# Performance work log

Hardware: AMD Instinct MI355X
Metric: run time of the kernel (lower is better)

The kernel has to match this reference:

```python
import jax, jax.numpy as jnp
import numpy as np

D_MODEL = 256
D_STATE = 16
D_CONV = 3
D_INNER = 512   # expand(2.0) * d_model
DT_RANK = 16    # ceil(d_model / 16)
BATCH = 4
SEQLEN = 2048


def setup_inputs() -> dict:
    key = jax.random.key(0)
    ks = jax.random.split(key, 8)
    s = 0.02
    x = jax.random.normal(ks[0], (BATCH, D_MODEL, SEQLEN), jnp.float32)
    W_in = jax.random.normal(ks[1], (2 * D_INNER, D_MODEL), jnp.float32) * s
    W_dw = jax.random.normal(ks[2], (D_INNER, 1, D_CONV), jnp.float32) * 0.3
    b_dw = jnp.zeros((D_INNER,), jnp.float32)
    W_x = jax.random.normal(ks[3], (DT_RANK + 2 * D_STATE, D_INNER), jnp.float32) * s
    W_dt = jax.random.normal(ks[4], (D_INNER, DT_RANK), jnp.float32) * s
    # bias so softplus(delta) stays small/stable, like mamba dt init
    b_dt = jax.random.normal(ks[5], (D_INNER,), jnp.float32) * 0.5 - 4.0
    A_log = jnp.log(jnp.broadcast_to(
        jnp.arange(1, D_STATE + 1, dtype=jnp.float32), (D_INNER, D_STATE)))
    D = jnp.ones((D_INNER,), jnp.float32)
    W_out = jax.random.normal(ks[6], (D_MODEL, D_INNER), jnp.float32) * s
    return {"x": x, "W_in": W_in, "W_dw": W_dw, "b_dw": b_dw, "W_x": W_x,
            "W_dt": W_dt, "b_dt": b_dt, "A_log": A_log, "D": D, "W_out": W_out}


def reference(x, W_in, W_dw, b_dw, W_x, W_dt, b_dt, A_log, D, W_out):
    residual = x
    # in_proj: 1x1 conv == per-position GEMM -> (B, 2*d_inner, L)
    xz = jnp.einsum('cd,bdl->bcl', W_in, x)
    u, z = jnp.split(xz, 2, axis=1)                       # each (B, d_inner, L)
    # depthwise conv1d, 'same' padding (pad = d_conv//2)
    u = jax.lax.conv_general_dilated(
        u, W_dw, window_strides=(1,), padding=[(D_CONV // 2, D_CONV // 2)],
        dimension_numbers=('NCH', 'OIH', 'NCH'), feature_group_count=D_INNER)
    u = jax.nn.silu(u + b_dw[None, :, None])
    # x_proj -> dt (low rank), B_ssm, C_ssm
    x_dbl = jnp.einsum('cd,bdl->bcl', W_x, u)             # (B, dt_rank+2N, L)
    dt_lr = x_dbl[:, :DT_RANK]                            # (B, dt_rank, L)
    B_ssm = x_dbl[:, DT_RANK:DT_RANK + D_STATE]           # (B, N, L)
    C_ssm = x_dbl[:, DT_RANK + D_STATE:]                  # (B, N, L)
    delta = jax.nn.softplus(
        jnp.einsum('dr,brl->bdl', W_dt, dt_lr) + b_dt[None, :, None])
    A = -jnp.exp(A_log)                                   # (d_inner, N)
    # discretized transition / input, laid out scan-major: (L, B, d_inner, N)
    dA = jnp.exp(jnp.einsum('bdl,dn->lbdn', delta, A))
    dBu = jnp.einsum('bdl,bnl,bdl->lbdn', delta, B_ssm, u)
    C_t = jnp.transpose(C_ssm, (2, 0, 1))                 # (L, B, N)
    h0 = jnp.zeros((x.shape[0], D_INNER, D_STATE), jnp.float32)

    def step(h, inp):
        dA_t, dBu_t, c_t = inp
        h = dA_t * h + dBu_t                              # (B, d_inner, N)
        y_t = jnp.einsum('bdn,bn->bd', h, c_t)            # (B, d_inner)
        return h, y_t

    _, ys = jax.lax.scan(step, h0, (dA, dBu, C_t))        # ys: (L, B, d_inner)
    y = jnp.transpose(ys, (1, 2, 0)) + D[None, :, None] * u
    y = y * jax.nn.silu(z)
    return jnp.einsum('od,bdl->bol', W_out, y) + residual
```

## Files before the change

### kernel.cpp

```cpp
#include <hip/hip_runtime.h>
#include <math.h>

#define DM 256
#define DI 512
#define BB 4
#define LL 2048
#define NC 64
#define CH (LL / NC)

typedef short bf16x8 __attribute__((ext_vector_type(8)));
typedef float f32x4 __attribute__((ext_vector_type(4)));
typedef unsigned short u16;

__device__ inline u16 f2bf(float f) {
    union { float f; unsigned u; } v;
    v.f = f;
    return (u16)((v.u + 0x7FFF + ((v.u >> 16) & 1)) >> 16);
}
__device__ inline float bf2f(u16 h) {
    union { unsigned u; float f; } v;
    v.u = ((unsigned)h) << 16;
    return v.f;
}

__global__ __launch_bounds__(256) void k_prep(const float* __restrict__ x,
                                              const float* __restrict__ W_in,
                                              const float* __restrict__ W_out,
                                              const float* __restrict__ W_x,
                                              u16* __restrict__ xt,
                                              u16* __restrict__ wbf_in,
                                              u16* __restrict__ wbf_out,
                                              u16* __restrict__ wbf_x) {
    const int bid = blockIdx.x;
    const int t = threadIdx.x;
    if (bid < 512) {
        __shared__ float tile[64][65];
        const int lb = bid & 31, mb = (bid >> 5) & 3, b = bid >> 7;
        const int m0 = mb * 64, l0 = lb * 64;
        const float* xb = x + ((size_t)b * DM + m0) * LL + l0;
#pragma unroll
        for (int i = 0; i < 16; i++) {
            int idx = t + i * 256;
            int r = idx >> 6, c = idx & 63;
            tile[r][c] = xb[(size_t)r * LL + c];
        }
        __syncthreads();
        u16* ob = xt + ((size_t)b * LL + l0) * DM + m0;
#pragma unroll
        for (int i = 0; i < 16; i++) {
            int idx = t + i * 256;
            int r = idx >> 6, c = idx & 63;
            ob[(size_t)r * DM + c] = f2bf(tile[c][r]);
        }
        return;
    }
    const float* src;
    u16* dst;
    int i4;
    if (bid < 768) { src = W_in; dst = wbf_in; i4 = (bid - 512) * 256 + t; }
    else if (bid < 896) { src = W_out; dst = wbf_out; i4 = (bid - 768) * 256 + t; }
    else { src = W_x; dst = wbf_x; i4 = (bid - 896) * 256 + t; }
    float4 v = ((const float4*)src)[i4];
    unsigned o0 = (unsigned)f2bf(v.x) | ((unsigned)f2bf(v.y) << 16);
    unsigned o1 = (unsigned)f2bf(v.z) | ((unsigned)f2bf(v.w) << 16);
    ((uint2*)dst)[i4] = make_uint2(o0, o1);
}

__global__ __launch_bounds__(256) void k_gemm_in(const u16* __restrict__ xt,
                                                 const u16* __restrict__ Wb,
                                                 u16* __restrict__ xz) {
    __shared__ short As[128 * 64];
    __shared__ short Bs[128 * 64];
    const int b = blockIdx.z;
    const int l0 = blockIdx.x * 128;
    const int c0 = blockIdx.y * 128;
    const int t = threadIdx.x;
    const int lane = t & 63, wv = t >> 6;
    const int wr = wv >> 1, wc = wv & 1;
    const u16* xb = xt + (size_t)b * LL * DM;
    f32x4 acc[4][4] = {};
    for (int k0 = 0; k0 < DM; k0 += 64) {
#pragma unroll
        for (int i = 0; i < 4; i++) {
            int ci = t + i * 256;
            int r = ci >> 3;
            int cb = (ci & 7) * 16;
            int pd = r * 128 + (cb ^ ((r & 7) << 4));
            *(float4*)((char*)As + pd) =
                *(const float4*)((const char*)(xb + (size_t)(l0 + r) * DM + k0) + cb);
            *(float4*)((char*)Bs + pd) =
                *(const float4*)((const char*)(Wb + (size_t)(c0 + r) * DM + k0) + cb);
        }
        __syncthreads();
#pragma unroll
        for (int kk = 0; kk < 2; kk++) {
            const int lcb = kk * 64 + (lane >> 4) * 16;
            bf16x8 af[4], bfr[4];
#pragma unroll
            for (int mi = 0; mi < 4; mi++) {
                int r = wr * 64 + mi * 16 + (lane & 15);
                af[mi] = *(const bf16x8*)((const char*)As + r * 128 + (lcb ^ ((r & 7) << 4)));
            }
#pragma unroll
            for (int ni = 0; ni < 4; ni++) {
                int r = wc * 64 + ni * 16 + (lane & 15);
                bfr[ni] = *(const bf16x8*)((const char*)Bs + r * 128 + (lcb ^ ((r & 7) << 4)));
            }
#pragma unroll
            for (int mi = 0; mi < 4; mi++)
#pragma unroll
                for (int ni = 0; ni < 4; ni++)
                    acc[mi][ni] = __builtin_amdgcn_mfma_f32_16x16x32_bf16(
                        af[mi], bfr[ni], acc[mi][ni], 0, 0, 0);
        }
        __syncthreads();
    }
    u16* ob = xz + (size_t)b * LL * 1024;
#pragma unroll
    for (int mi = 0; mi < 4; mi++) {
#pragma unroll
        for (int q = 0; q < 4; q++) {
            int l = l0 + wr * 64 + mi * 16 + (lane >> 4) * 4 + q;
#pragma unroll
            for (int ni = 0; ni < 4; ni++) {
                int c = c0 + wc * 64 + ni * 16 + (lane & 15);
                ob[(size_t)l * 1024 + c] = f2bf(acc[mi][ni][q]);
            }
        }
    }
}

__global__ __launch_bounds__(256) void k_conv(const u16* __restrict__ xz,
                                              const float* __restrict__ Wdw,
                                              const float* __restrict__ bdw,
                                              u16* __restrict__ u_bf) {
    int idx = blockIdx.x * 256 + threadIdx.x;
    int g = idx & 63;
    int l = (idx >> 6) & (LL - 1);
    int b = idx >> 17;
    int d0 = g * 8;
    const u16* row = xz + ((size_t)b * LL + l) * 1024 + d0;
    ushort4 c0a = *(const ushort4*)(row);
    ushort4 c0b = *(const ushort4*)(row + 4);
    ushort4 cma, cmb, cpa, cpb;
    if (l > 0) { cma = *(const ushort4*)(row - 1024); cmb = *(const ushort4*)(row - 1020); }
    else { cma = make_ushort4(0, 0, 0, 0); cmb = cma; }
    if (l < LL - 1) { cpa = *(const ushort4*)(row + 1024); cpb = *(const ushort4*)(row + 1028); }
    else { cpa = make_ushort4(0, 0, 0, 0); cpb = cpa; }
    u16 xm[8] = {cma.x, cma.y, cma.z, cma.w, cmb.x, cmb.y, cmb.z, cmb.w};
    u16 x0[8] = {c0a.x, c0a.y, c0a.z, c0a.w, c0b.x, c0b.y, c0b.z, c0b.w};
    u16 xp[8] = {cpa.x, cpa.y, cpa.z, cpa.w, cpb.x, cpb.y, cpb.z, cpb.w};
    u16 out[8];
#pragma unroll
    for (int j = 0; j < 8; j++) {
        int d = d0 + j;
        float v = bdw[d] + Wdw[d * 3] * bf2f(xm[j]) + Wdw[d * 3 + 1] * bf2f(x0[j]) +
                  Wdw[d * 3 + 2] * bf2f(xp[j]);
        float uu = v / (1.f + __expf(-v));
        out[j] = f2bf(uu);
    }
    u16* ou = u_bf + ((size_t)b * LL + l) * DI + d0;
    *(ushort4*)(ou) = make_ushort4(out[0], out[1], out[2], out[3]);
    *(ushort4*)(ou + 4) = make_ushort4(out[4], out[5], out[6], out[7]);
}

__global__ __launch_bounds__(256) void k_xdbl(const u16* __restrict__ u_bf,
                                              const u16* __restrict__ Wxb,
                                              float* __restrict__ xdbl_p) {
    __shared__ short Us[64 * 64];
    __shared__ short Ws[48 * 64];
    const int bl0 = (blockIdx.x >> 2) * 64;
    const int kp = blockIdx.x & 3;
    const int t = threadIdx.x;
    const int lane = t & 63, wv = t >> 6;
    f32x4 acc[3] = {};
#pragma unroll
    for (int ks = 0; ks < 2; ks++) {
        const int k0 = kp * 128 + ks * 64;
        if (ks) __syncthreads();
#pragma unroll
        for (int i = 0; i < 2; i++) {
            int ci = t + i * 256;
            int r = ci >> 3;
            int cb = (ci & 7) * 16;
            int pd = r * 128 + (cb ^ ((r & 7) << 4));
            *(float4*)((char*)Us + pd) =
                *(const float4*)((const char*)(u_bf + (size_t)(bl0 + r) * DI + k0) + cb);
            if (ci < 384)
                *(float4*)((char*)Ws + pd) =
                    *(const float4*)((const char*)(Wxb + (size_t)r * DI + k0) + cb);
        }
        __syncthreads();
#pragma unroll
        for (int kk = 0; kk < 2; kk++) {
            int lcb = kk * 64 + (lane >> 4) * 16;
            int ra = wv * 16 + (lane & 15);
            bf16x8 af = *(const bf16x8*)((const char*)Us + ra * 128 + (lcb ^ ((ra & 7) << 4)));
#pragma unroll
            for (int ni = 0; ni < 3; ni++) {
                int r2 = ni * 16 + (lane & 15);
                bf16x8 bfr = *(const bf16x8*)((const char*)Ws + r2 * 128 + (lcb ^ ((r2 & 7) << 4)));
                acc[ni] = __builtin_amdgcn_mfma_f32_16x16x32_bf16(af, bfr, acc[ni], 0, 0, 0);
            }
        }
    }
#pragma unroll
    for (int ni = 0; ni < 3; ni++)
#pragma unroll
        for (int q = 0; q < 4; q++) {
            int l = bl0 + wv * 16 + (lane >> 4) * 4 + q;
            int c = ni * 16 + (lane & 15);
            xdbl_p[((size_t)kp * BB * LL + l) * 48 + c] = acc[ni][q];
        }
}

__global__ __launch_bounds__(256) void k_delta(const float* __restrict__ xdbl_p,
                                               const float* __restrict__ Wdt,
                                               const float* __restrict__ bdt,
                                               float* __restrict__ xdbl,
                                               u16* __restrict__ delta_bf) {
    __shared__ float xd[16][52];
    const int bl0 = blockIdx.x * 16;
    const int t = threadIdx.x;
#pragma unroll
    for (int i = 0; i < 3; i++) {
        int idx = t + i * 256;
        int l = idx / 48, c = idx - l * 48;
        size_t off = (size_t)(bl0 + l) * 48 + c;
        float s = xdbl_p[off] + xdbl_p[(size_t)BB * LL * 48 + off] +
                  xdbl_p[(size_t)2 * BB * LL * 48 + off] +
                  xdbl_p[(size_t)3 * BB * LL * 48 + off];
        xd[l][c] = s;
        xdbl[off] = s;
    }
    __syncthreads();
    float wr0[16], wr1[16];
    {
        const float4* wp0 = (const float4*)(Wdt + (size_t)t * 16);
        const float4* wp1 = (const float4*)(Wdt + (size_t)(t + 256) * 16);
#pragma unroll
        for (int q = 0; q < 4; q++) {
            float4 w = wp0[q];
            wr0[q * 4] = w.x; wr0[q * 4 + 1] = w.y; wr0[q * 4 + 2] = w.z; wr0[q * 4 + 3] = w.w;
            float4 u = wp1[q];
            wr1[q * 4] = u.x; wr1[q * 4 + 1] = u.y; wr1[q * 4 + 2] = u.z; wr1[q * 4 + 3] = u.w;
        }
    }
    const float b0 = bdt[t], b1 = bdt[t + 256];
#pragma unroll 4
    for (int ll = 0; ll < 16; ll++) {
        float a0 = b0, a1 = b1;
#pragma unroll
        for (int q = 0; q < 4; q++) {
            f32x4 xv = *(const f32x4*)&xd[ll][q * 4];
#pragma unroll
            for (int j = 0; j < 4; j++) {
                a0 += wr0[q * 4 + j] * xv[j];
                a1 += wr1[q * 4 + j] * xv[j];
            }
        }
        float sp0 = fmaxf(a0, 0.f) + __logf(1.f + __expf(-fabsf(a0)));
        float sp1 = fmaxf(a1, 0.f) + __logf(1.f + __expf(-fabsf(a1)));
        delta_bf[(size_t)(bl0 + ll) * DI + t] = f2bf(sp0);
        delta_bf[(size_t)(bl0 + ll) * DI + t + 256] = f2bf(sp1);
    }
}

__global__ __launch_bounds__(256) void k_scanA(const u16* __restrict__ delta_bf,
                                               const float* __restrict__ xdbl,
                                               const u16* __restrict__ u_bf,
                                               const float* __restrict__ A_log,
                                               u16* __restrict__ hend,
                                               float* __restrict__ dsum) {
    const int t = threadIdx.x;
    const int d = blockIdx.y * 256 + t;
    const int b = blockIdx.z;
    const int c = blockIdx.x;
    const int l0 = c * CH;
    const size_t bl0 = (size_t)b * LL + l0;
    float Av[16];
    bool fast = true;
    {
        const float4* Ar = (const float4*)(A_log + (size_t)d * 16);
#pragma unroll
        for (int q = 0; q < 4; q++) {
            float4 a = Ar[q];
            Av[q * 4] = -__expf(a.x); Av[q * 4 + 1] = -__expf(a.y);
            Av[q * 4 + 2] = -__expf(a.z); Av[q * 4 + 3] = -__expf(a.w);
        }
#pragma unroll
        for (int n = 0; n < 16; n++)
            fast = fast && (fabsf(Av[n] + (float)(n + 1)) < 1e-4f * (n + 1));
    }
    const u16* dl = delta_bf + bl0 * DI + d;
    const u16* ul = u_bf + bl0 * DI + d;
    const float* Bg = xdbl + bl0 * 48 + 16;
    float h[16] = {};
    float ds = 0.f;
#pragma unroll 4
    for (int s = 0; s < CH; s++) {
        float de = bf2f(dl[(size_t)s * DI]);
        float uu = bf2f(ul[(size_t)s * DI]);
        float du = de * uu;
        ds += de;
        float pw[16];
        if (fast) {
            float p1 = __expf(-de);
            float p2 = p1 * p1, p4 = p2 * p2, p8 = p4 * p4;
            pw[0] = p1; pw[1] = p2; pw[2] = p2 * p1; pw[3] = p4;
            pw[4] = p4 * p1; pw[5] = p4 * p2; pw[6] = p4 * pw[2]; pw[7] = p8;
            pw[8] = p8 * p1; pw[9] = p8 * p2; pw[10] = p8 * pw[2]; pw[11] = p8 * p4;
            pw[12] = p8 * pw[4]; pw[13] = p8 * pw[5]; pw[14] = p8 * pw[6]; pw[15] = p8 * p8;
        } else {
#pragma unroll
            for (int n = 0; n < 16; n++) pw[n] = __expf(de * Av[n]);
        }
#pragma unroll
        for (int q = 0; q < 4; q++) {
            f32x4 Bv = *(const f32x4*)(Bg + (size_t)s * 48 + q * 4);
#pragma unroll
            for (int j = 0; j < 4; j++) {
                int n = q * 4 + j;
                h[n] = pw[n] * h[n] + du * Bv[j];
            }
        }
    }
    size_t base = ((size_t)b * NC + c) * DI + d;
#pragma unroll
    for (int n = 0; n < 16; n++) hend[base * 16 + n] = f2bf(h[n]);
    dsum[base] = ds;
}

__global__ __launch_bounds__(256) void k_scanB(const float* __restrict__ A_log,
                                               const float* __restrict__ dsum,
                                               const u16* __restrict__ hend,
                                               u16* __restrict__ hinit) {
    int idx = blockIdx.x * 256 + threadIdx.x;
    int n = idx & 15;
    int d = (idx >> 4) & 511;
    int b = idx >> 13;
    float Av = -__expf(A_log[d * 16 + n]);
    float h = 0.f;
#pragma unroll 8
    for (int c = 0; c < NC; c++) {
        size_t base = ((size_t)b * NC + c) * DI + d;
        hinit[base * 16 + n] = f2bf(h);
        h = __expf(dsum[base] * Av) * h + bf2f(hend[base * 16 + n]);
    }
}

__global__ __launch_bounds__(256) void k_scanC(const u16* __restrict__ delta_bf,
                                               const float* __restrict__ xdbl,
                                               const u16* __restrict__ u_bf,
                                               const u16* __restrict__ xz,
                                               const float* __restrict__ A_log,
                                               const float* __restrict__ Dp,
                                               const u16* __restrict__ hinit,
                                               u16* __restrict__ y_bf) {
    const int t = threadIdx.x;
    const int d = blockIdx.y * 256 + t;
    const int b = blockIdx.z;
    const int c = blockIdx.x;
    const int l0 = c * CH;
    const size_t bl0 = (size_t)b * LL + l0;
    float Av[16];
    bool fast = true;
    {
        const float4* Ar = (const float4*)(A_log + (size_t)d * 16);
#pragma unroll
        for (int q = 0; q < 4; q++) {
            float4 a = Ar[q];
            Av[q * 4] = -__expf(a.x); Av[q * 4 + 1] = -__expf(a.y);
            Av[q * 4 + 2] = -__expf(a.z); Av[q * 4 + 3] = -__expf(a.w);
        }
#pragma unroll
        for (int n = 0; n < 16; n++)
            fast = fast && (fabsf(Av[n] + (float)(n + 1)) < 1e-4f * (n + 1));
    }
    float h[16];
    {
        size_t base = ((size_t)b * NC + c) * DI + d;
#pragma unroll
        for (int n = 0; n < 16; n++) h[n] = bf2f(hinit[base * 16 + n]);
    }
    const u16* dl = delta_bf + bl0 * DI + d;
    const u16* ul = u_bf + bl0 * DI + d;
    const u16* zl = xz + bl0 * 1024 + 512 + d;
    u16* yl = y_bf + bl0 * DI + d;
    const float* Bg = xdbl + bl0 * 48 + 16;
    const float* Cg = xdbl + bl0 * 48 + 32;
    const float Dv = Dp[d];
#pragma unroll 4
    for (int s = 0; s < CH; s++) {
        float de = bf2f(dl[(size_t)s * DI]);
        float uu = bf2f(ul[(size_t)s * DI]);
        float zz = bf2f(zl[(size_t)s * 1024]);
        float du = de * uu;
        float pw[16];
        if (fast) {
            float p1 = __expf(-de);
            float p2 = p1 * p1, p4 = p2 * p2, p8 = p4 * p4;
            pw[0] = p1; pw[1] = p2; pw[2] = p2 * p1; pw[3] = p4;
            pw[4] = p4 * p1; pw[5] = p4 * p2; pw[6] = p4 * pw[2]; pw[7] = p8;
            pw[8] = p8 * p1; pw[9] = p8 * p2; pw[10] = p8 * pw[2]; pw[11] = p8 * p4;
            pw[12] = p8 * pw[4]; pw[13] = p8 * pw[5]; pw[14] = p8 * pw[6]; pw[15] = p8 * p8;
        } else {
#pragma unroll
            for (int n = 0; n < 16; n++) pw[n] = __expf(de * Av[n]);
        }
        float dot = 0.f;
#pragma unroll
        for (int q = 0; q < 4; q++) {
            f32x4 Bv = *(const f32x4*)(Bg + (size_t)s * 48 + q * 4);
            f32x4 Cv = *(const f32x4*)(Cg + (size_t)s * 48 + q * 4);
#pragma unroll
            for (int j = 0; j < 4; j++) {
                int n = q * 4 + j;
                h[n] = pw[n] * h[n] + du * Bv[j];
                dot += h[n] * Cv[j];
            }
        }
        float sig = 1.f / (1.f + __expf(-zz));
        yl[(size_t)s * DI] = f2bf((dot + Dv * uu) * (zz * sig));
    }
}

__global__ __launch_bounds__(256) void k_gemm_out(const u16* __restrict__ Wb,
                                                  const u16* __restrict__ yb,
                                                  const float* __restrict__ x,
                                                  float* __restrict__ out) {
    __shared__ short As[64 * 64];
    __shared__ short Bs[128 * 64];
    const int b = blockIdx.z;
    const int l0 = blockIdx.x * 128;
    const int o0 = blockIdx.y * 64;
    const int t = threadIdx.x;
    const int lane = t & 63, wv = t >> 6;
    const u16* ybb = yb + (size_t)b * LL * DI;
    f32x4 acc[4][2] = {};
    for (int k0 = 0; k0 < DI; k0 += 64) {
#pragma unroll
        for (int i = 0; i < 2; i++) {
            int ci = t + i * 256;
            int r = ci >> 3;
            int cb = (ci & 7) * 16;
            int pd = r * 128 + (cb ^ ((r & 7) << 4));
            *(float4*)((char*)As + pd) =
                *(const float4*)((const char*)(Wb + (size_t)(o0 + r) * DI + k0) + cb);
        }
#pragma unroll
        for (int i = 0; i < 4; i++) {
            int ci = t + i * 256;
            int r = ci >> 3;
            int cb = (ci & 7) * 16;
            int pd = r * 128 + (cb ^ ((r & 7) << 4));
            *(float4*)((char*)Bs + pd) =
                *(const float4*)((const char*)(ybb + (size_t)(l0 + r) * DI + k0) + cb);
        }
        __syncthreads();
#pragma unroll
        for (int kk = 0; kk < 2; kk++) {
            const int lcb = kk * 64 + (lane >> 4) * 16;
            bf16x8 af[4], bfr[2];
#pragma unroll
            for (int mi = 0; mi < 4; mi++) {
                int r = mi * 16 + (lane & 15);
                af[mi] = *(const bf16x8*)((const char*)As + r * 128 + (lcb ^ ((r & 7) << 4)));
            }
#pragma unroll
            for (int ni = 0; ni < 2; ni++) {
                int r = wv * 32 + ni * 16 + (lane & 15);
                bfr[ni] = *(const bf16x8*)((const char*)Bs + r * 128 + (lcb ^ ((r & 7) << 4)));
            }
#pragma unroll
            for (int mi = 0; mi < 4; mi++)
#pragma unroll
                for (int ni = 0; ni < 2; ni++)
                    acc[mi][ni] = __builtin_amdgcn_mfma_f32_16x16x32_bf16(
                        af[mi], bfr[ni], acc[mi][ni], 0, 0, 0);
        }
        __syncthreads();
    }
#pragma unroll
    for (int mi = 0; mi < 4; mi++) {
#pragma unroll
        for (int q = 0; q < 4; q++) {
            int o = o0 + mi * 16 + (lane >> 4) * 4 + q;
#pragma unroll
            for (int ni = 0; ni < 2; ni++) {
                int l = l0 + wv * 32 + ni * 16 + (lane & 15);
                size_t a = ((size_t)b * DM + o) * LL + l;
                out[a] = acc[mi][ni][q] + x[a];
            }
        }
    }
}

extern "C" void kernel_launch(void* const* d_in, const int* in_sizes, int n_in,
                              void* d_out, int out_size, void* d_ws, size_t ws_size,
                              hipStream_t stream) {
    const float* x = (const float*)d_in[0];
    const float* W_in = (const float*)d_in[1];
    const float* W_dw = (const float*)d_in[2];
    const float* b_dw = (const float*)d_in[3];
    const float* W_x = (const float*)d_in[4];
    const float* W_dt = (const float*)d_in[5];
    const float* b_dt = (const float*)d_in[6];
    const float* A_log = (const float*)d_in[7];
    const float* Dp = (const float*)d_in[8];
    const float* W_out = (const float*)d_in[9];
    float* out = (float*)d_out;

    char* p = (char*)d_ws;
    u16* xz_bf = (u16*)p;      p += (size_t)BB * LL * 1024 * 2;
    u16* u_bf = (u16*)p;       p += (size_t)BB * LL * DI * 2;
    u16* delta_bf = (u16*)p;   p += (size_t)BB * LL * DI * 2;
    float* xdbl = (float*)p;   p += (size_t)BB * LL * 48 * 4;
    float* xdbl_p = (float*)p; p += (size_t)4 * BB * LL * 48 * 4;
    u16* y_bf = (u16*)p;       p += (size_t)BB * LL * DI * 2;
    float* dsum = (float*)p;   p += (size_t)BB * NC * DI * 4;
    u16* hinit = (u16*)p;      p += (size_t)BB * NC * DI * 16 * 2;
    u16* wbf_in = (u16*)p;     p += (size_t)2 * DI * DM * 2;
    u16* wbf_out = (u16*)p;    p += (size_t)DM * DI * 2;
    u16* wbf_x = (u16*)p;      p += (size_t)48 * DI * 2;
    u16* xt = delta_bf;
    u16* hend = y_bf;

    k_prep<<<920, 256, 0, stream>>>(x, W_in, W_out, W_x, xt, wbf_in, wbf_out, wbf_x);
    k_gemm_in<<<dim3(LL / 128, 1024 / 128, BB), 256, 0, stream>>>(xt, wbf_in, xz_bf);
    k_conv<<<(BB * LL * 64) / 256, 256, 0, stream>>>(xz_bf, W_dw, b_dw, u_bf);
    k_xdbl<<<(BB * LL / 64) * 4, 256, 0, stream>>>(u_bf, wbf_x, xdbl_p);
    k_delta<<<BB * LL / 16, 256, 0, stream>>>(xdbl_p, W_dt, b_dt, xdbl, delta_bf);
    k_scanA<<<dim3(NC, DI / 256, BB), 256, 0, stream>>>(delta_bf, xdbl, u_bf, A_log,
                                                        hend, dsum);
    k_scanB<<<(BB * DI * 16) / 256, 256, 0, stream>>>(A_log, dsum, hend, hinit);
    k_scanC<<<dim3(NC, DI / 256, BB), 256, 0, stream>>>(delta_bf, xdbl, u_bf, xz_bf,
                                                        A_log, Dp, hinit, y_bf);
    k_gemm_out<<<dim3(LL / 128, DM / 64, BB), 256, 0, stream>>>(wbf_out, y_bf, x, out);
}
```

Before: 93.52 us.

## Use direct global-to-LDS loads in GEMM staging and double scan chunk count

Replaces the register-staged global→LDS tile copies in the three GEMM kernels with the global_load_lds builtin. The swizzle is applied on the global read side so that each wave writes contiguous 8-row blocks into LDS. This is meant to skip the VGPR round trip and the separate ds_write instructions. It also raises the scan chunk count from 64 to 128, giving more parallelism in the chunked scan at the cost of more inter-chunk state to combine.

After: 87.02 us. 1.07x faster.

```diff
diff --git a/kernel.cpp b/kernel.cpp
--- a/kernel.cpp
+++ b/kernel.cpp
@@ -5,7 +5,7 @@
 #define DI 512
 #define BB 4
 #define LL 2048
-#define NC 64
+#define NC 128
 #define CH (LL / NC)
 
 typedef short bf16x8 __attribute__((ext_vector_type(8)));
@@ -21,6 +21,14 @@
     union { unsigned u; float f; } v;
     v.u = ((unsigned)h) << 16;
     return v.f;
+}
+
+__device__ inline void gload_lds16(const void* g, void* l) {
+    auto* gp = reinterpret_cast<const __attribute__((address_space(1))) unsigned int*>(
+        reinterpret_cast<uintptr_t>(g));
+    auto* lp = reinterpret_cast<__attribute__((address_space(3))) unsigned int*>(
+        reinterpret_cast<uintptr_t>(l));
+    __builtin_amdgcn_global_load_lds(gp, lp, 16, 0, 0);
 }
 
 __global__ __launch_bounds__(256) void k_prep(const float* __restrict__ x,
@@ -77,19 +85,19 @@
     const int t = threadIdx.x;
     const int lane = t & 63, wv = t >> 6;
     const int wr = wv >> 1, wc = wv & 1;
+    const int rsub = lane >> 3;
+    const int colb = ((lane & 7) * 16) ^ ((rsub & 7) << 4);
     const u16* xb = xt + (size_t)b * LL * DM;
     f32x4 acc[4][4] = {};
     for (int k0 = 0; k0 < DM; k0 += 64) {
 #pragma unroll
         for (int i = 0; i < 4; i++) {
-            int ci = t + i * 256;
-            int r = ci >> 3;
-            int cb = (ci & 7) * 16;
-            int pd = r * 128 + (cb ^ ((r & 7) << 4));
-            *(float4*)((char*)As + pd) =
-                *(const float4*)((const char*)(xb + (size_t)(l0 + r) * DM + k0) + cb);
-            *(float4*)((char*)Bs + pd) =
-                *(const float4*)((const char*)(Wb + (size_t)(c0 + r) * DM + k0) + cb);
+            int rb = wv * 32 + i * 8;
+            int r = rb + rsub;
+            gload_lds16((const char*)(xb + (size_t)(l0 + r) * DM + k0) + colb,
+                        (char*)As + rb * 128);
+            gload_lds16((const char*)(Wb + (size_t)(c0 + r) * DM + k0) + colb,
+                        (char*)Bs + rb * 128);
         }
         __syncthreads();
 #pragma unroll
@@ -173,6 +181,8 @@
     const int kp = blockIdx.x & 3;
     const int t = threadIdx.x;
     const int lane = t & 63, wv = t >> 6;
+    const int rsub = lane >> 3;
+    const int colb = ((lane & 7) * 16) ^ ((rsub & 7) << 4);
     f32x4 acc[3] = {};
 #pragma unroll
     for (int ks = 0; ks < 2; ks++) {
@@ -180,15 +190,13 @@
         if (ks) __syncthreads();
 #pragma unroll
         for (int i = 0; i < 2; i++) {
-            int ci = t + i * 256;
-            int r = ci >> 3;
-            int cb = (ci & 7) * 16;
-            int pd = r * 128 + (cb ^ ((r & 7) << 4));
-            *(float4*)((char*)Us + pd) =
-                *(const float4*)((const char*)(u_bf + (size_t)(bl0 + r) * DI + k0) + cb);
-            if (ci < 384)
-                *(float4*)((char*)Ws + pd) =
-                    *(const float4*)((const char*)(Wxb + (size_t)r * DI + k0) + cb);
+            int rb = wv * 16 + i * 8;
+            int r = rb + rsub;
+            gload_lds16((const char*)(u_bf + (size_t)(bl0 + r) * DI + k0) + colb,
+                        (char*)Us + rb * 128);
+            if (wv < 3)
+                gload_lds16((const char*)(Wxb + (size_t)r * DI + k0) + colb,
+                            (char*)Ws + rb * 128);
         }
         __syncthreads();
 #pragma unroll
@@ -436,26 +444,24 @@
     const int o0 = blockIdx.y * 64;
     const int t = threadIdx.x;
     const int lane = t & 63, wv = t >> 6;
+    const int rsub = lane >> 3;
+    const int colb = ((lane & 7) * 16) ^ ((rsub & 7) << 4);
     const u16* ybb = yb + (size_t)b * LL * DI;
     f32x4 acc[4][2] = {};
     for (int k0 = 0; k0 < DI; k0 += 64) {
 #pragma unroll
         for (int i = 0; i < 2; i++) {
-            int ci = t + i * 256;
-            int r = ci >> 3;
-            int cb = (ci & 7) * 16;
-            int pd = r * 128 + (cb ^ ((r & 7) << 4));
-            *(float4*)((char*)As + pd) =
-                *(const float4*)((const char*)(Wb + (size_t)(o0 + r) * DI + k0) + cb);
+            int rb = wv * 16 + i * 8;
+            int r = rb + rsub;
+            gload_lds16((const char*)(Wb + (size_t)(o0 + r) * DI + k0) + colb,
+                        (char*)As + rb * 128);
         }
 #pragma unroll
         for (int i = 0; i < 4; i++) {
-            int ci = t + i * 256;
-            int r = ci >> 3;
-            int cb = (ci & 7) * 16;
-            int pd = r * 128 + (cb ^ ((r & 7) << 4));
-            *(float4*)((char*)Bs + pd) =
-                *(const float4*)((const char*)(ybb + (size_t)(l0 + r) * DI + k0) + cb);
+            int rb = wv * 32 + i * 8;
+            int r = rb + rsub;
+            gload_lds16((const char*)(ybb + (size_t)(l0 + r) * DI + k0) + colb,
+                        (char*)Bs + rb * 128);
         }
         __syncthreads();
 #pragma unroll
```
